# Optimization experiments

Measured on AMD Instinct MI355X. Metric: run time of the kernel, lower is better.

## Reference

```python
import jax, jax.numpy as jnp
import numpy as np

N_ATOMS = 700_000   # total atoms, sorted by degree
K = 7               # nb_affine = max_deg + 1 - min_deg (degrees 0..6)
PER_DEG = 100_000   # atoms per degree bucket
B = 2048            # batch_size (molecules)
F = 128             # n_atom_features
C = 128             # nb_filter


def setup_inputs() -> dict:
    key = jax.random.key(0)
    k_atoms, k_mem, k_adj, k_w = jax.random.split(key, 4)
    atoms = jax.random.normal(k_atoms, (N_ATOMS, F), dtype=jnp.float32)
    # contiguous degree-sorted layout: degree d occupies rows [d*PER_DEG, (d+1)*PER_DEG)
    deg_slice = jnp.stack(
        [jnp.arange(K, dtype=jnp.int32) * PER_DEG,
         jnp.full((K,), PER_DEG, dtype=jnp.int32)], axis=1)
    membership = jax.random.randint(k_mem, (N_ATOMS,), 0, B, dtype=jnp.int32)
    adj = {f"deg_adj_{d}": jax.random.randint(jax.random.fold_in(k_adj, d),
                                               (PER_DEG, d), 0, N_ATOMS, dtype=jnp.int32)
           for d in range(1, K)}
    W = jax.random.normal(k_w, (K, F, C), dtype=jnp.float32) * 0.05
    b = jnp.zeros((K, C), dtype=jnp.float32)  # model_ops.zeros init
    return dict(atoms=atoms, deg_slice=deg_slice, membership=membership,
                W=W, b=b, **adj)


def reference(atoms, deg_slice, membership, W, b,
              deg_adj_1, deg_adj_2, deg_adj_3, deg_adj_4, deg_adj_5, deg_adj_6):
    # deg_adj_* are dead inputs in the original graph (sum_neigh result is unused).
    n_atoms = atoms.shape[0]
    k = W.shape[0]
    # per-atom degree id from contiguous deg_slice (atoms sorted by degree)
    deg_per_atom = jnp.repeat(jnp.arange(k, dtype=jnp.int32), deg_slice[:, 1],
                              total_repeat_length=n_atoms)
    # weight-iterator order: degree d>=1 -> W[d-1], degree 0 -> W[k-1]
    widx = jnp.where(deg_per_atom == 0, k - 1, deg_per_atom - 1)
    # molecule-level readout: sum_i (atoms[i] @ W[widx_i] + b[widx_i]) grouped by membership
    # = sum_k (segment_sum of atoms per (mol, widx)) @ W[k] + counts @ b
    seg = membership.astype(jnp.int32) * k + widx  # (n_atoms,) in [0, B*k)
    S = jax.ops.segment_sum(atoms, seg, num_segments=B * k).reshape(B, k, -1)
    cnt = jax.ops.segment_sum(jnp.ones((n_atoms,), atoms.dtype), seg,
                              num_segments=B * k).reshape(B, k)
    out = jnp.einsum('bkf,kfc->bc', S, W) + cnt @ b  # (B, C)
    return out  # activation is 'linear', dropout is None
```

## Files before the change

### kernel.cpp

```cpp
#include <hip/hip_runtime.h>

#define N_ATOMS  700000
#define PER_DEG  100000
#define KDEG     7
#define NB       2048
#define NF       128
#define NSEG     (NB * KDEG)

#define WS_CNT      0
#define WS_CURSOR   (WS_CNT + NSEG)
#define WS_OFFSETS  (WS_CURSOR + NSEG)
#define WS_PERM     43024
#define WS_S        (WS_PERM + N_ATOMS)

typedef float vfloat4 __attribute__((ext_vector_type(4)));

__device__ __forceinline__ int widx_of(int i) {
    int d = i / PER_DEG;
    return (d == 0) ? (KDEG - 1) : (d - 1);
}

__global__ void hist_kernel(const int* __restrict__ mem, int* __restrict__ cnt) {
    int i = blockIdx.x * blockDim.x + threadIdx.x;
    if (i < N_ATOMS) {
        int seg = mem[i] * KDEG + widx_of(i);
        atomicAdd(&cnt[seg], 1);
    }
}

__global__ void scan_kernel(const int* __restrict__ cnt,
                            int* __restrict__ offsets,
                            int* __restrict__ cursor) {
    __shared__ int part[1024];
    int t = threadIdx.x;
    int base = t * 14;
    int local[14];
    int sum = 0;
#pragma unroll
    for (int i = 0; i < 14; ++i) { local[i] = cnt[base + i]; sum += local[i]; }
    part[t] = sum;
    __syncthreads();
    for (int off = 1; off < 1024; off <<= 1) {
        int v = (t >= off) ? part[t - off] : 0;
        __syncthreads();
        part[t] += v;
        __syncthreads();
    }
    int run = (t == 0) ? 0 : part[t - 1];
#pragma unroll
    for (int i = 0; i < 14; ++i) {
        offsets[base + i] = run;
        cursor[base + i]  = run;
        run += local[i];
    }
    if (t == 1023) offsets[NSEG] = run;
}

__global__ void scatter_kernel(const int* __restrict__ mem,
                               int* __restrict__ cursor,
                               int* __restrict__ perm) {
    int i = blockIdx.x * blockDim.x + threadIdx.x;
    if (i < N_ATOMS) {
        int seg = mem[i] * KDEG + widx_of(i);
        int pos = atomicAdd(&cursor[seg], 1);
        perm[pos] = i;
    }
}

__global__ __launch_bounds__(128) void segsum_kernel(
        const float* __restrict__ atoms,
        const int* __restrict__ perm,
        const int* __restrict__ offsets,
        float* __restrict__ S) {
    int s = blockIdx.x;
    int t = threadIdx.x;
    int g = t >> 5;
    int l = t & 31;
    int beg = offsets[s];
    int end = offsets[s + 1];

    vfloat4 acc0 = {0.f, 0.f, 0.f, 0.f};
    vfloat4 acc1 = {0.f, 0.f, 0.f, 0.f};
    vfloat4 acc2 = {0.f, 0.f, 0.f, 0.f};
    vfloat4 acc3 = {0.f, 0.f, 0.f, 0.f};

    int j = beg;
    int i0 = 0, i1 = 0, i2 = 0, i3 = 0;
    if (j + 16 <= end) {
        i0 = perm[j + g];      i1 = perm[j + 4 + g];
        i2 = perm[j + 8 + g];  i3 = perm[j + 12 + g];
    }
    while (j + 16 <= end) {
        int jn = j + 16;
        int n0 = i0, n1 = i1, n2 = i2, n3 = i3;
        if (jn + 16 <= end) {
            n0 = perm[jn + g];      n1 = perm[jn + 4 + g];
            n2 = perm[jn + 8 + g];  n3 = perm[jn + 12 + g];
        }
        const vfloat4* p0 = (const vfloat4*)(atoms + (size_t)i0 * NF);
        const vfloat4* p1 = (const vfloat4*)(atoms + (size_t)i1 * NF);
        const vfloat4* p2 = (const vfloat4*)(atoms + (size_t)i2 * NF);
        const vfloat4* p3 = (const vfloat4*)(atoms + (size_t)i3 * NF);
        vfloat4 v0 = __builtin_nontemporal_load(p0 + l);
        vfloat4 v1 = __builtin_nontemporal_load(p1 + l);
        vfloat4 v2 = __builtin_nontemporal_load(p2 + l);
        vfloat4 v3 = __builtin_nontemporal_load(p3 + l);
        acc0 += v0;
        acc1 += v1;
        acc2 += v2;
        acc3 += v3;
        i0 = n0; i1 = n1; i2 = n2; i3 = n3;
        j = jn;
    }
    if (j + 8 <= end) {
        int r0 = perm[j + g];
        int r1 = perm[j + 4 + g];
        const vfloat4* p0 = (const vfloat4*)(atoms + (size_t)r0 * NF);
        const vfloat4* p1 = (const vfloat4*)(atoms + (size_t)r1 * NF);
        acc0 += __builtin_nontemporal_load(p0 + l);
        acc1 += __builtin_nontemporal_load(p1 + l);
        j += 8;
    }
    for (; j < end; j += 4) {
        int r = j + g;
        if (r < end) {
            int row = perm[r];
            const vfloat4* p = (const vfloat4*)(atoms + (size_t)row * NF);
            acc0 += __builtin_nontemporal_load(p + l);
        }
    }
    acc0 += acc1;
    acc2 += acc3;
    acc0 += acc2;

    __shared__ vfloat4 red[128];
    red[t] = acc0;
    __syncthreads();
    if (t < 32) {
        vfloat4 o = red[t] + red[t + 32] + red[t + 64] + red[t + 96];
        ((vfloat4*)(S + (size_t)s * NF))[l] = o;
    }
}

__global__ __launch_bounds__(256) void gemm_kernel(
        const float* __restrict__ S,
        const int* __restrict__ cnt,
        const float* __restrict__ W,
        const float* __restrict__ b,
        float* __restrict__ out) {
    __shared__ float sS[8][KDEG * NF];
    int m0 = blockIdx.x * 8;
    int t = threadIdx.x;
    int c = t & 127;
    int g = t >> 7;

    for (int idx = t; idx < 8 * KDEG * NF; idx += 256) {
        int mm = idx / (KDEG * NF);
        int ff = idx - mm * (KDEG * NF);
        sS[mm][ff] = S[(size_t)(m0 + mm) * (KDEG * NF) + ff];
    }
    __syncthreads();

    int mb = g * 4;
    float a0 = 0.f, a1 = 0.f, a2 = 0.f, a3 = 0.f;
#pragma unroll 8
    for (int kf = 0; kf < KDEG * NF; ++kf) {
        float w = W[kf * 128 + c];
        a0 += sS[mb + 0][kf] * w;
        a1 += sS[mb + 1][kf] * w;
        a2 += sS[mb + 2][kf] * w;
        a3 += sS[mb + 3][kf] * w;
    }
    float acc[4] = {a0, a1, a2, a3};
#pragma unroll
    for (int i = 0; i < 4; ++i) {
        int m = m0 + mb + i;
        float bias = 0.f;
#pragma unroll
        for (int k = 0; k < KDEG; ++k)
            bias += (float)cnt[m * KDEG + k] * b[k * 128 + c];
        out[(size_t)m * 128 + c] = acc[i] + bias;
    }
}

extern "C" void kernel_launch(void* const* d_in, const int* in_sizes, int n_in,
                              void* d_out, int out_size, void* d_ws, size_t ws_size,
                              hipStream_t stream) {
    const float* atoms      = (const float*)d_in[0];
    const int*   membership = (const int*)d_in[2];
    const float* W          = (const float*)d_in[3];
    const float* bvec       = (const float*)d_in[4];
    float* out = (float*)d_out;

    int*   ws_i = (int*)d_ws;
    int*   cnt     = ws_i + WS_CNT;
    int*   cursor  = ws_i + WS_CURSOR;
    int*   offsets = ws_i + WS_OFFSETS;
    int*   perm    = ws_i + WS_PERM;
    float* S       = (float*)d_ws + WS_S;

    hipMemsetAsync(cnt, 0, NSEG * sizeof(int), stream);

    int nblk = (N_ATOMS + 255) / 256;
    hist_kernel<<<nblk, 256, 0, stream>>>(membership, cnt);
    scan_kernel<<<1, 1024, 0, stream>>>(cnt, offsets, cursor);
    scatter_kernel<<<nblk, 256, 0, stream>>>(membership, cursor, perm);
    segsum_kernel<<<NSEG, 128, 0, stream>>>(atoms, perm, offsets, S);
    gemm_kernel<<<NB / 8, 256, 0, stream>>>(S, cnt, W, bvec, out);
}
```

Before: 593.8 us.

## Fuse segment-sum and GEMM into one persistent cooperative kernel

Merges the segment-sum and GEMM kernels into a single cooperative launch. A persistent grid strides over segments, does a grid-wide sync, then strides over molecule groups of 4 for the GEMM. This saves one kernel launch and the tail between the two kernels. In exchange the GEMM tile shrinks to 4 molecules per 128-thread block, the persistent grid loses some latency hiding in the gather, and the grid sync adds its own cost.

```diff
diff --git a/kernel.cpp b/kernel.cpp
--- a/kernel.cpp
+++ b/kernel.cpp
@@ -1,4 +1,7 @@
 #include <hip/hip_runtime.h>
+#include <hip/hip_cooperative_groups.h>
+
+namespace cg = cooperative_groups;
 
 #define N_ATOMS  700000
 #define PER_DEG  100000
@@ -67,119 +70,116 @@
     }
 }
 
-__global__ __launch_bounds__(128) void segsum_kernel(
+__global__ __launch_bounds__(128, 4) void fused_kernel(
         const float* __restrict__ atoms,
-        const int* __restrict__ perm,
-        const int* __restrict__ offsets,
-        float* __restrict__ S) {
-    int s = blockIdx.x;
+        const int*   __restrict__ perm,
+        const int*   __restrict__ offsets,
+        const int*   __restrict__ cnt,
+        const float* __restrict__ W,
+        const float* __restrict__ b,
+        float* __restrict__ S,
+        float* __restrict__ out) {
+    __shared__ vfloat4 red[128];
+    __shared__ float   sS[4][KDEG * NF];
+
     int t = threadIdx.x;
     int g = t >> 5;
     int l = t & 31;
-    int beg = offsets[s];
-    int end = offsets[s + 1];
-
-    vfloat4 acc0 = {0.f, 0.f, 0.f, 0.f};
-    vfloat4 acc1 = {0.f, 0.f, 0.f, 0.f};
-    vfloat4 acc2 = {0.f, 0.f, 0.f, 0.f};
-    vfloat4 acc3 = {0.f, 0.f, 0.f, 0.f};
-
-    int j = beg;
-    int i0 = 0, i1 = 0, i2 = 0, i3 = 0;
-    if (j + 16 <= end) {
-        i0 = perm[j + g];      i1 = perm[j + 4 + g];
-        i2 = perm[j + 8 + g];  i3 = perm[j + 12 + g];
-    }
-    while (j + 16 <= end) {
-        int jn = j + 16;
-        int n0 = i0, n1 = i1, n2 = i2, n3 = i3;
-        if (jn + 16 <= end) {
-            n0 = perm[jn + g];      n1 = perm[jn + 4 + g];
-            n2 = perm[jn + 8 + g];  n3 = perm[jn + 12 + g];
-        }
-        const vfloat4* p0 = (const vfloat4*)(atoms + (size_t)i0 * NF);
-        const vfloat4* p1 = (const vfloat4*)(atoms + (size_t)i1 * NF);
-        const vfloat4* p2 = (const vfloat4*)(atoms + (size_t)i2 * NF);
-        const vfloat4* p3 = (const vfloat4*)(atoms + (size_t)i3 * NF);
-        vfloat4 v0 = __builtin_nontemporal_load(p0 + l);
-        vfloat4 v1 = __builtin_nontemporal_load(p1 + l);
-        vfloat4 v2 = __builtin_nontemporal_load(p2 + l);
-        vfloat4 v3 = __builtin_nontemporal_load(p3 + l);
-        acc0 += v0;
-        acc1 += v1;
-        acc2 += v2;
-        acc3 += v3;
-        i0 = n0; i1 = n1; i2 = n2; i3 = n3;
-        j = jn;
-    }
-    if (j + 8 <= end) {
-        int r0 = perm[j + g];
-        int r1 = perm[j + 4 + g];
-        const vfloat4* p0 = (const vfloat4*)(atoms + (size_t)r0 * NF);
-        const vfloat4* p1 = (const vfloat4*)(atoms + (size_t)r1 * NF);
-        acc0 += __builtin_nontemporal_load(p0 + l);
-        acc1 += __builtin_nontemporal_load(p1 + l);
-        j += 8;
-    }
-    for (; j < end; j += 4) {
-        int r = j + g;
-        if (r < end) {
-            int row = perm[r];
-            const vfloat4* p = (const vfloat4*)(atoms + (size_t)row * NF);
-            acc0 += __builtin_nontemporal_load(p + l);
-        }
-    }
-    acc0 += acc1;
-    acc2 += acc3;
-    acc0 += acc2;
-
-    __shared__ vfloat4 red[128];
-    red[t] = acc0;
-    __syncthreads();
-    if (t < 32) {
-        vfloat4 o = red[t] + red[t + 32] + red[t + 64] + red[t + 96];
-        ((vfloat4*)(S + (size_t)s * NF))[l] = o;
-    }
-}
-
-__global__ __launch_bounds__(256) void gemm_kernel(
-        const float* __restrict__ S,
-        const int* __restrict__ cnt,
-        const float* __restrict__ W,
-        const float* __restrict__ b,
-        float* __restrict__ out) {
-    __shared__ float sS[8][KDEG * NF];
-    int m0 = blockIdx.x * 8;
-    int t = threadIdx.x;
-    int c = t & 127;
-    int g = t >> 7;
-
-    for (int idx = t; idx < 8 * KDEG * NF; idx += 256) {
-        int mm = idx / (KDEG * NF);
-        int ff = idx - mm * (KDEG * NF);
-        sS[mm][ff] = S[(size_t)(m0 + mm) * (KDEG * NF) + ff];
-    }
-    __syncthreads();
-
-    int mb = g * 4;
-    float a0 = 0.f, a1 = 0.f, a2 = 0.f, a3 = 0.f;
+
+    for (int s = blockIdx.x; s < NSEG; s += gridDim.x) {
+        int beg = offsets[s];
+        int end = offsets[s + 1];
+
+        vfloat4 acc0 = {0.f, 0.f, 0.f, 0.f};
+        vfloat4 acc1 = {0.f, 0.f, 0.f, 0.f};
+        vfloat4 acc2 = {0.f, 0.f, 0.f, 0.f};
+        vfloat4 acc3 = {0.f, 0.f, 0.f, 0.f};
+
+        int j = beg;
+        int i0 = 0, i1 = 0, i2 = 0, i3 = 0;
+        if (j + 16 <= end) {
+            i0 = perm[j + g];      i1 = perm[j + 4 + g];
+            i2 = perm[j + 8 + g];  i3 = perm[j + 12 + g];
+        }
+        while (j + 16 <= end) {
+            int jn = j + 16;
+            int n0 = i0, n1 = i1, n2 = i2, n3 = i3;
+            if (jn + 16 <= end) {
+                n0 = perm[jn + g];      n1 = perm[jn + 4 + g];
+                n2 = perm[jn + 8 + g];  n3 = perm[jn + 12 + g];
+            }
+            const vfloat4* p0 = (const vfloat4*)(atoms + (size_t)i0 * NF);
+            const vfloat4* p1 = (const vfloat4*)(atoms + (size_t)i1 * NF);
+            const vfloat4* p2 = (const vfloat4*)(atoms + (size_t)i2 * NF);
+            const vfloat4* p3 = (const vfloat4*)(atoms + (size_t)i3 * NF);
+            acc0 += __builtin_nontemporal_load(p0 + l);
+            acc1 += __builtin_nontemporal_load(p1 + l);
+            acc2 += __builtin_nontemporal_load(p2 + l);
+            acc3 += __builtin_nontemporal_load(p3 + l);
+            i0 = n0; i1 = n1; i2 = n2; i3 = n3;
+            j = jn;
+        }
+        if (j + 8 <= end) {
+            int r0 = perm[j + g];
+            int r1 = perm[j + 4 + g];
+            const vfloat4* p0 = (const vfloat4*)(atoms + (size_t)r0 * NF);
+            const vfloat4* p1 = (const vfloat4*)(atoms + (size_t)r1 * NF);
+            acc0 += __builtin_nontemporal_load(p0 + l);
+            acc1 += __builtin_nontemporal_load(p1 + l);
+            j += 8;
+        }
+        for (; j < end; j += 4) {
+            int r = j + g;
+            if (r < end) {
+                int row = perm[r];
+                const vfloat4* p = (const vfloat4*)(atoms + (size_t)row * NF);
+                acc0 += __builtin_nontemporal_load(p + l);
+            }
+        }
+        acc0 += acc1;
+        acc2 += acc3;
+        acc0 += acc2;
+
+        red[t] = acc0;
+        __syncthreads();
+        if (t < 32) {
+            vfloat4 o = red[t] + red[t + 32] + red[t + 64] + red[t + 96];
+            ((vfloat4*)(S + (size_t)s * NF))[l] = o;
+        }
+        __syncthreads();
+    }
+
+    cg::this_grid().sync();
+
+    for (int m0 = blockIdx.x * 4; m0 < NB; m0 += gridDim.x * 4) {
+        for (int idx = t; idx < 4 * KDEG * NF; idx += 128) {
+            int mm = idx / (KDEG * NF);
+            int ff = idx - mm * (KDEG * NF);
+            sS[mm][ff] = S[(size_t)(m0 + mm) * (KDEG * NF) + ff];
+        }
+        __syncthreads();
+
+        int c = t;
+        float a0 = 0.f, a1 = 0.f, a2 = 0.f, a3 = 0.f;
 #pragma unroll 8
-    for (int kf = 0; kf < KDEG * NF; ++kf) {
-        float w = W[kf * 128 + c];
-        a0 += sS[mb + 0][kf] * w;
-        a1 += sS[mb + 1][kf] * w;
-        a2 += sS[mb + 2][kf] * w;
-        a3 += sS[mb + 3][kf] * w;
-    }
-    float acc[4] = {a0, a1, a2, a3};
-#pragma unroll
-    for (int i = 0; i < 4; ++i) {
-        int m = m0 + mb + i;
-        float bias = 0.f;
-#pragma unroll
-        for (int k = 0; k < KDEG; ++k)
-            bias += (float)cnt[m * KDEG + k] * b[k * 128 + c];
-        out[(size_t)m * 128 + c] = acc[i] + bias;
+        for (int kf = 0; kf < KDEG * NF; ++kf) {
+            float w = W[kf * 128 + c];
+            a0 += sS[0][kf] * w;
+            a1 += sS[1][kf] * w;
+            a2 += sS[2][kf] * w;
+            a3 += sS[3][kf] * w;
+        }
+        float acc[4] = {a0, a1, a2, a3};
+#pragma unroll
+        for (int i = 0; i < 4; ++i) {
+            int m = m0 + i;
+            float bias = 0.f;
+#pragma unroll
+            for (int k = 0; k < KDEG; ++k)
+                bias += (float)cnt[m * KDEG + k] * b[k * 128 + c];
+            out[(size_t)m * 128 + c] = acc[i] + bias;
+        }
+        __syncthreads();
     }
 }
 
@@ -205,6 +205,20 @@
     hist_kernel<<<nblk, 256, 0, stream>>>(membership, cnt);
     scan_kernel<<<1, 1024, 0, stream>>>(cnt, offsets, cursor);
     scatter_kernel<<<nblk, 256, 0, stream>>>(membership, cursor, perm);
-    segsum_kernel<<<NSEG, 128, 0, stream>>>(atoms, perm, offsets, S);
-    gemm_kernel<<<NB / 8, 256, 0, stream>>>(S, cnt, W, bvec, out);
-}
+
+    static int coop_blocks = 0;
+    if (coop_blocks == 0) {
+        int per_cu = 0;
+        hipError_t e = hipOccupancyMaxActiveBlocksPerMultiprocessor(
+            &per_cu, (const void*)fused_kernel, 128, 0);
+        if (e != hipSuccess || per_cu <= 0) per_cu = 1;
+        long total = (long)per_cu * 256;
+        if (total > 2048) total = 2048;
+        coop_blocks = (int)total;
+    }
+    void* args[] = { (void*)&atoms, (void*)&perm, (void*)&offsets,
+                     (void*)&cnt, (void*)&W, (void*)&bvec,
+                     (void*)&S, (void*)&out };
+    hipLaunchCooperativeKernel((void*)fused_kernel, dim3(coop_blocks),
+                               dim3(128), args, 0, stream);
+}
```

Result: slower. 800.7 us (+34.8%).
